# Optimization experiments

Measured on AMD Instinct MI355X. Metric: run time of the kernel, lower is better.

The kernel has to match this reference:

```python
import jax, jax.numpy as jnp
import numpy as np

EMB = 128
BINS = 32
CUT = 5.0
NLAYER = 5
NHID = 4  # extra hidden linears in edge MLP (hidden_dim_list has 5 entries total)
N_NODES = 50000
N_EDGES = 800000
N_GRAPH = 256
NODE_CLASS = 100


def setup_inputs() -> dict:
    key = jax.random.key(0)
    ks = jax.random.split(key, 20)
    s = 0.02
    inp = {
        'z': jax.random.randint(ks[0], (N_NODES,), 0, NODE_CLASS),
        'pos': jax.random.normal(ks[1], (N_NODES, 3), dtype=jnp.float32) * 3.0,
        'batch': jnp.sort(jax.random.randint(ks[2], (N_NODES,), 0, N_GRAPH)),
        'edge_index': jax.random.randint(ks[3], (2, N_EDGES), 0, N_NODES),
        # parameters
        'atom_table': jax.random.normal(ks[4], (NODE_CLASS, EMB), dtype=jnp.float32) * s,
        'atom_w': jax.random.normal(ks[5], (EMB, EMB), dtype=jnp.float32) * s,
        'atom_b': jnp.zeros((EMB,), jnp.float32),
        'edge_emb_w': jax.random.normal(ks[6], (BINS, EMB), dtype=jnp.float32) * s,
        'edge_emb_b': jnp.zeros((EMB,), jnp.float32),
        'edge_w0': jax.random.normal(ks[7], (NLAYER, 3 * EMB, EMB), dtype=jnp.float32) * s,
        'edge_b0': jnp.zeros((NLAYER, EMB), jnp.float32),
        'edge_w': jax.random.normal(ks[8], (NLAYER, NHID, EMB, EMB), dtype=jnp.float32) * s,
        'edge_b': jnp.zeros((NLAYER, NHID, EMB), jnp.float32),
        'node_w': jax.random.normal(ks[9], (NLAYER, EMB, EMB), dtype=jnp.float32) * s,
        'node_b': jnp.zeros((NLAYER, EMB), jnp.float32),
        'out_w': jax.random.normal(ks[10], (EMB, 1), dtype=jnp.float32) * s,
        'out_b': jnp.zeros((1,), jnp.float32),
    }
    return inp


def reference(z, pos, batch, edge_index, atom_table, atom_w, atom_b,
              edge_emb_w, edge_emb_b, edge_w0, edge_b0, edge_w, edge_b,
              node_w, node_b, out_w, out_b):
    silu = jax.nn.silu
    row, col = edge_index[0], edge_index[1]

    # atom embedding + linear
    h_node = atom_table[z] @ atom_w + atom_b  # [N, EMB]

    # edge distances -> gaussian basis expansion (linear spacing, log_base=1.0)
    d = jnp.linalg.norm(pos[row] - pos[col], axis=-1)  # [E]
    mu = jnp.linspace(0.0, CUT, BINS, dtype=jnp.float32)
    sigma = CUT / BINS
    basis = jnp.exp(-0.5 * ((d[:, None] - mu) / sigma) ** 2)  # [E, BINS]
    h_edge = basis @ edge_emb_w + edge_emb_b  # [E, EMB]

    # message passing layers
    for l in range(NLAYER):
        m = jnp.concatenate([h_edge, h_node[row], h_node[col]], axis=-1)  # [E, 3*EMB]
        m = silu(m @ edge_w0[l] + edge_b0[l])
        for k in range(NHID):
            m = silu(m @ edge_w[l, k] + edge_b[l, k])
        h_edge = h_edge + m  # residual edge update
        agg = jax.ops.segment_sum(h_edge, row, num_segments=N_NODES)  # [N, EMB]
        h_node = h_node + silu(agg @ node_w[l] + node_b[l])  # residual node update

    # scatter-mean graph pool
    sums = jax.ops.segment_sum(h_node, batch, num_segments=N_GRAPH)
    cnt = jax.ops.segment_sum(jnp.ones((h_node.shape[0],), h_node.dtype), batch, num_segments=N_GRAPH)
    h_graph = sums / jnp.clip(cnt, 1.0)[:, None]

    return h_graph @ out_w + out_b  # [N_GRAPH, 1]
```

## Files before the change

### kernel.cpp

```cpp
#include <hip/hip_runtime.h>

#define EMB      128
#define N_NODES_ 50000
#define N_EDGES_ 800000
#define N_GRAPH_ 256
#define NLAYER_  5

#define WP_ATOM  573440
#define WP_NODE0 589824
#define WP_EMB   671744
#define WP_TOTAL 675840

typedef short short8 __attribute__((ext_vector_type(8)));
typedef float floatx4 __attribute__((ext_vector_type(4)));

__device__ __forceinline__ float silu_f(float x) {
    return __fdividef(x, 1.0f + __expf(-x));
}
__device__ __forceinline__ float bf2f(unsigned short h) {
    return __uint_as_float(((unsigned)h) << 16);
}
__device__ __forceinline__ unsigned short f2bf(float f) {
    unsigned u = __float_as_uint(f);
    unsigned r = 0x7FFFu + ((u >> 16) & 1u);
    return (unsigned short)((u + r) >> 16);
}

#if defined(__has_builtin)
#if __has_builtin(__builtin_amdgcn_cvt_pk_bf16_f32)
#define HAVE_PK_BF16 1
#endif
#endif
#ifdef HAVE_PK_BF16
typedef __bf16 bf16x2 __attribute__((ext_vector_type(2)));
__device__ __forceinline__ unsigned f2bf_pk(float a, float b) {
    bf16x2 v = __builtin_amdgcn_cvt_pk_bf16_f32(a, b);
    unsigned u;
    __builtin_memcpy(&u, &v, 4);
    return u;
}
#else
__device__ __forceinline__ unsigned f2bf_pk(float a, float b) {
    return (unsigned)f2bf(a) | ((unsigned)f2bf(b) << 16);
}
#endif

__device__ __forceinline__ void wave_lds_fence() {
    __builtin_amdgcn_fence(__ATOMIC_ACQ_REL, "wavefront");
    __builtin_amdgcn_wave_barrier();
}

__global__ __launch_bounds__(256) void hist_kernel(
    const int* __restrict__ row, int* __restrict__ hist)
{
    const int e = blockIdx.x * 256 + threadIdx.x;
    if (e < N_EDGES_) atomicAdd(&hist[row[e]], 1);
}

__global__ __launch_bounds__(256) void scan_kernel(
    const int* __restrict__ hist, int* __restrict__ cursor)
{
    __shared__ int ssum[256];
    const int tid = threadIdx.x;
    const int chunk = (N_NODES_ + 255) / 256;
    const int base = tid * chunk;
    int s = 0;
    for (int i = 0; i < chunk; ++i) {
        const int idx = base + i;
        if (idx < N_NODES_) s += hist[idx];
    }
    ssum[tid] = s;
    __syncthreads();
    for (int off = 1; off < 256; off <<= 1) {
        const int t2 = (tid >= off) ? ssum[tid - off] : 0;
        __syncthreads();
        ssum[tid] += t2;
        __syncthreads();
    }
    int run = ssum[tid] - s;
    for (int i = 0; i < chunk; ++i) {
        const int idx = base + i;
        if (idx < N_NODES_) { cursor[idx] = run; run += hist[idx]; }
    }
}

__global__ __launch_bounds__(256) void scatter_kernel(
    const int* __restrict__ row, const int* __restrict__ col,
    int* __restrict__ cursor, int* __restrict__ row_s, int* __restrict__ col_s)
{
    const int e = blockIdx.x * 256 + threadIdx.x;
    if (e >= N_EDGES_) return;
    const int r = row[e];
    const int p = atomicAdd(&cursor[r], 1);
    row_s[p] = r;
    col_s[p] = col[e];
}

__global__ __launch_bounds__(256) void pack_w_kernel(
    const float* __restrict__ edge_w0, const float* __restrict__ edge_w,
    const float* __restrict__ atom_w, const float* __restrict__ node_w,
    const float* __restrict__ edge_emb_w,
    unsigned short* __restrict__ Wp)
{
    const int bid = blockIdx.x;
    int Kb, t;
    const float* src;
    unsigned short* dst;
    if (bid < 200) {
        const int l = bid / 40, r = bid % 40, s = r / 8;
        t = r % 8;
        Kb = (s == 0) ? 12 : 4;
        src = (s == 0) ? edge_w0 + (size_t)l * 384 * 128
                       : edge_w + ((size_t)l * 4 + (s - 1)) * 128 * 128;
        dst = Wp + (size_t)l * 114688 + ((s == 0) ? 0 : (49152 + (s - 1) * 16384))
            + (size_t)t * Kb * 512;
    } else if (bid < 208) {
        t = bid - 200; Kb = 4; src = atom_w;
        dst = Wp + WP_ATOM + (size_t)t * Kb * 512;
    } else if (bid < 248) {
        const int l = (bid - 208) >> 3; t = (bid - 208) & 7; Kb = 4;
        src = node_w + (size_t)l * 128 * 128;
        dst = Wp + WP_NODE0 + (size_t)l * 16384 + (size_t)t * Kb * 512;
    } else {
        t = bid - 248; Kb = 1; src = edge_emb_w;
        dst = Wp + WP_EMB + (size_t)t * 512;
    }
    const int n = Kb * 512;
    for (int p = threadIdx.x; p < n; p += 256) {
        const int j = p & 7, lane = (p >> 3) & 63, kb = p >> 9;
        const int k  = kb * 32 + ((lane >> 4) << 3) + j;
        const int nn = t * 16 + (lane & 15);
        dst[p] = f2bf(src[(size_t)k * 128 + nn]);
    }
}

__global__ __launch_bounds__(256, 3) void edge_mlp_csr_kernel(
    const unsigned short* __restrict__ h_node_bf, unsigned short* __restrict__ h_edge,
    const int* __restrict__ row_s, const int* __restrict__ col_s,
    const unsigned short* __restrict__ Wp,
    const float* __restrict__ b0, const float* __restrict__ bh)
{
    __shared__ __align__(16) unsigned short A[64][392];
    const int tid = threadIdx.x;
    const int e0 = blockIdx.x * 64;

    short8 he_reg[4];

    {
        const int t = tid >> 2, q = tid & 3;
        const int rg = row_s[e0 + t];
        const int cg = col_s[e0 + t];
        const unsigned short* pe = &h_edge[(size_t)(e0 + t) * 128];
        const unsigned short* pr = &h_node_bf[(size_t)rg * 128];
        const unsigned short* pc = &h_node_bf[(size_t)cg * 128];
#pragma unroll
        for (int i = 0; i < 12; ++i) {
            const int ch = q + 4 * i;
            const int k8 = ch << 3;
            const unsigned short* src = (ch < 16) ? (pe + k8)
                                      : (ch < 32) ? (pr + (k8 - 128))
                                                  : (pc + (k8 - 256));
            const short8 v = *(const short8*)src;
            if (i < 4) he_reg[i] = v;
            *(short8*)&A[t][k8] = v;
        }
    }
    __syncthreads();

    const int lane = tid & 63;
    const int wv   = tid >> 6;
    const int lr   = lane & 15;
    const int lg   = lane >> 4;
    const int nt0  = 2 * wv, nt1 = nt0 + 1;

    for (int s = 0; s < 5; ++s) {
        const int Kb   = (s == 0) ? 12 : 4;
        const int inb  = (s == 0) ? 0 : ((s & 1) ? 128 : 0);
        const int outb = (s & 1) ? 0 : 128;
        const unsigned short* __restrict__ Ws =
            Wp + ((s == 0) ? 0 : (49152 + (s - 1) * 16384));
        const float* __restrict__ bias = (s == 0) ? b0 : (bh + (s - 1) * 128);

        const float4 bv0 = *(const float4*)&bias[nt0 * 16 + lg * 4];
        const float4 bv1 = *(const float4*)&bias[nt1 * 16 + lg * 4];
        floatx4 acc0[4], acc1[4];
#pragma unroll
        for (int et = 0; et < 4; ++et) {
            acc0[et] = (floatx4){bv0.x, bv0.y, bv0.z, bv0.w};
            acc1[et] = (floatx4){bv1.x, bv1.y, bv1.z, bv1.w};
        }

        const unsigned short* aptr0 = Ws + ((size_t)(nt0 * Kb) * 64 + lane) * 8;
        const unsigned short* aptr1 = Ws + ((size_t)(nt1 * Kb) * 64 + lane) * 8;
#pragma unroll 2
        for (int kb = 0; kb < Kb; ++kb) {
            const short8 wf0 = *(const short8*)(aptr0 + (size_t)kb * 512);
            const short8 wf1 = *(const short8*)(aptr1 + (size_t)kb * 512);
#pragma unroll
            for (int et = 0; et < 4; ++et) {
                const short8 mf = *(const short8*)&A[et * 16 + lr][inb + kb * 32 + lg * 8];
                acc0[et] = __builtin_amdgcn_mfma_f32_16x16x32_bf16(wf0, mf, acc0[et], 0, 0, 0);
                acc1[et] = __builtin_amdgcn_mfma_f32_16x16x32_bf16(wf1, mf, acc1[et], 0, 0, 0);
            }
        }
        if (s == 0) __syncthreads();
#pragma unroll
        for (int et = 0; et < 4; ++et) {
            uint2 p0, p1;
            p0.x = f2bf_pk(silu_f(acc0[et][0]), silu_f(acc0[et][1]));
            p0.y = f2bf_pk(silu_f(acc0[et][2]), silu_f(acc0[et][3]));
            p1.x = f2bf_pk(silu_f(acc1[et][0]), silu_f(acc1[et][1]));
            p1.y = f2bf_pk(silu_f(acc1[et][2]), silu_f(acc1[et][3]));
            *(uint2*)&A[et * 16 + lr][outb + nt0 * 16 + lg * 4] = p0;
            *(uint2*)&A[et * 16 + lr][outb + nt1 * 16 + lg * 4] = p1;
        }
        __syncthreads();
    }

    {
        const int t = tid >> 2, q = tid & 3;
        unsigned short* pe = &h_edge[(size_t)(e0 + t) * 128];
#pragma unroll
        for (int i = 0; i < 4; ++i) {
            const int k8 = (q + 4 * i) << 3;
            const short8 mv = *(const short8*)&A[t][128 + k8];
            const short8 ov = he_reg[i];
            float he[8];
#pragma unroll
            for (int j = 0; j < 8; ++j)
                he[j] = bf2f((unsigned short)ov[j]) + bf2f((unsigned short)mv[j]);
            uint4 sv;
            sv.x = f2bf_pk(he[0], he[1]);
            sv.y = f2bf_pk(he[2], he[3]);
            sv.z = f2bf_pk(he[4], he[5]);
            sv.w = f2bf_pk(he[6], he[7]);
            *(uint4*)(pe + k8) = sv;
        }
    }
}

__global__ __launch_bounds__(256, 4) void node_agg_gemm_kernel(
    const unsigned short* __restrict__ h_edge,
    const int* __restrict__ hist, const int* __restrict__ cur_end,
    const unsigned short* __restrict__ Wpm, const float* __restrict__ bias,
    unsigned short* __restrict__ h_node_bf, int N)
{
    __shared__ __align__(16) unsigned short B[64][136];
    const int tid  = threadIdx.x;
    const int lane = tid & 63;
    const int wv   = tid >> 6;
    const int n0   = blockIdx.x * 64;

    {
        const int t = tid >> 2, q = tid & 3;
        const int n = n0 + t;
        float a[32];
#pragma unroll
        for (int j = 0; j < 32; ++j) a[j] = 0.f;
        if (n < N) {
            const int e_end = cur_end[n];
            const int e_beg = e_end - hist[n];
            for (int e = e_beg; e < e_end; ++e) {
                const unsigned short* p = &h_edge[(size_t)e * 128 + q * 32];
#pragma unroll
                for (int g = 0; g < 4; ++g) {
                    const short8 v = *(const short8*)(p + g * 8);
#pragma unroll
                    for (int j = 0; j < 8; ++j)
                        a[g * 8 + j] += bf2f((unsigned short)v[j]);
                }
            }
        }
#pragma unroll
        for (int g = 0; g < 4; ++g) {
            uint4 pk;
            pk.x = f2bf_pk(a[g * 8 + 0], a[g * 8 + 1]);
            pk.y = f2bf_pk(a[g * 8 + 2], a[g * 8 + 3]);
            pk.z = f2bf_pk(a[g * 8 + 4], a[g * 8 + 5]);
            pk.w = f2bf_pk(a[g * 8 + 6], a[g * 8 + 7]);
            *(uint4*)&B[t][q * 32 + g * 8] = pk;
        }
    }
    wave_lds_fence();

    const int lr = lane & 15, lg = lane >> 4;
    floatx4 acc[8];
#pragma unroll
    for (int nt = 0; nt < 8; ++nt) {
        const float4 bv = *(const float4*)&bias[nt * 16 + lg * 4];
        acc[nt] = (floatx4){bv.x, bv.y, bv.z, bv.w};
    }
    const unsigned short* brow = &B[wv * 16 + lr][0];
#pragma unroll 2
    for (int kb = 0; kb < 4; ++kb) {
        const short8 mf = *(const short8*)(brow + kb * 32 + lg * 8);
#pragma unroll
        for (int nt = 0; nt < 8; ++nt) {
            const short8 wf = *(const short8*)(Wpm + ((size_t)(nt * 4 + kb) * 64 + lane) * 8);
            acc[nt] = __builtin_amdgcn_mfma_f32_16x16x32_bf16(wf, mf, acc[nt], 0, 0, 0);
        }
    }
    const int node = n0 + wv * 16 + lr;
    if (node < N) {
        unsigned short* drow = &h_node_bf[(size_t)node * 128];
#pragma unroll
        for (int nt = 0; nt < 8; ++nt) {
            float x0 = silu_f(acc[nt][0]), x1 = silu_f(acc[nt][1]);
            float x2 = silu_f(acc[nt][2]), x3 = silu_f(acc[nt][3]);
            unsigned short* p = drow + nt * 16 + lg * 4;
            const uint2 d = *(const uint2*)p;
            x0 += bf2f((unsigned short)(d.x & 0xFFFF));
            x1 += bf2f((unsigned short)(d.x >> 16));
            x2 += bf2f((unsigned short)(d.y & 0xFFFF));
            x3 += bf2f((unsigned short)(d.y >> 16));
            uint2 o;
            o.x = f2bf_pk(x0, x1);
            o.y = f2bf_pk(x2, x3);
            *(uint2*)p = o;
        }
    }
}

__global__ __launch_bounds__(256, 4) void atom_gemm_mfma_kernel(
    const float* __restrict__ src, const int* __restrict__ gidx,
    const unsigned short* __restrict__ Wpm, const float* __restrict__ bias,
    unsigned short* __restrict__ dst, int N)
{
    __shared__ __align__(16) unsigned short B[64][136];
    const int tid  = threadIdx.x;
    const int lane = tid & 63;
    const int wv   = tid >> 6;
    const int n0   = blockIdx.x * 64;

    {
        const int t = tid >> 2, q = tid & 3;
        const int node = n0 + t;
        const float* srow = src;
        if (node < N) srow = &src[(size_t)gidx[node] * 128];
#pragma unroll
        for (int i = 0; i < 4; ++i) {
            const int k8 = (q + 4 * i) << 3;
            uint4 pk = make_uint4(0, 0, 0, 0);
            if (node < N) {
                const float4 f0 = *(const float4*)(srow + k8);
                const float4 f1 = *(const float4*)(srow + k8 + 4);
                pk.x = f2bf_pk(f0.x, f0.y);
                pk.y = f2bf_pk(f0.z, f0.w);
                pk.z = f2bf_pk(f1.x, f1.y);
                pk.w = f2bf_pk(f1.z, f1.w);
            }
            *(uint4*)&B[t][k8] = pk;
        }
    }
    wave_lds_fence();

    const int lr = lane & 15, lg = lane >> 4;
    floatx4 acc[8];
#pragma unroll
    for (int nt = 0; nt < 8; ++nt) {
        const float4 bv = *(const float4*)&bias[nt * 16 + lg * 4];
        acc[nt] = (floatx4){bv.x, bv.y, bv.z, bv.w};
    }
    const unsigned short* brow = &B[wv * 16 + lr][0];
#pragma unroll 2
    for (int kb = 0; kb < 4; ++kb) {
        const short8 mf = *(const short8*)(brow + kb * 32 + lg * 8);
#pragma unroll
        for (int nt = 0; nt < 8; ++nt) {
            const short8 wf = *(const short8*)(Wpm + ((size_t)(nt * 4 + kb) * 64 + lane) * 8);
            acc[nt] = __builtin_amdgcn_mfma_f32_16x16x32_bf16(wf, mf, acc[nt], 0, 0, 0);
        }
    }
    const int node = n0 + wv * 16 + lr;
    if (node < N) {
        unsigned short* drow = &dst[(size_t)node * 128];
#pragma unroll
        for (int nt = 0; nt < 8; ++nt) {
            uint2 o;
            o.x = f2bf_pk(acc[nt][0], acc[nt][1]);
            o.y = f2bf_pk(acc[nt][2], acc[nt][3]);
            *(uint2*)(drow + nt * 16 + lg * 4) = o;
        }
    }
}

__global__ __launch_bounds__(256, 4) void edge_embed_mfma_kernel(
    const float* __restrict__ pos, const int* __restrict__ row, const int* __restrict__ col,
    const unsigned short* __restrict__ Wpe, const float* __restrict__ bemb,
    unsigned short* __restrict__ h_edge)
{
    __shared__ __align__(16) unsigned short Bas[64][40];
    const int tid  = threadIdx.x;
    const int lane = tid & 63;
    const int wv   = tid >> 6;
    const int e0   = blockIdx.x * 64;

    {
        const int t = tid >> 2, q = tid & 3;
        const int rr = row[e0 + t], cc = col[e0 + t];
        const float dx = pos[rr * 3 + 0] - pos[cc * 3 + 0];
        const float dy = pos[rr * 3 + 1] - pos[cc * 3 + 1];
        const float dz = pos[rr * 3 + 2] - pos[cc * 3 + 2];
        const float d = sqrtf(dx * dx + dy * dy + dz * dz);
        const float invs = 32.0f / 5.0f;
        float e[8];
#pragma unroll
        for (int j = 0; j < 8; ++j) {
            const float mu = (float)(q * 8 + j) * (5.0f / 31.0f);
            const float tt = (d - mu) * invs;
            e[j] = __expf(-0.5f * tt * tt);
        }
        uint4 pk;
        pk.x = f2bf_pk(e[0], e[1]);
        pk.y = f2bf_pk(e[2], e[3]);
        pk.z = f2bf_pk(e[4], e[5]);
        pk.w = f2bf_pk(e[6], e[7]);
        *(uint4*)&Bas[t][q * 8] = pk;
    }
    wave_lds_fence();

    const int lr = lane & 15, lg = lane >> 4;
    floatx4 acc[8];
#pragma unroll
    for (int nt = 0; nt < 8; ++nt) {
        const float4 bv = *(const float4*)&bemb[nt * 16 + lg * 4];
        acc[nt] = (floatx4){bv.x, bv.y, bv.z, bv.w};
    }
    const short8 mf = *(const short8*)&Bas[wv * 16 + lr][lg * 8];
#pragma unroll
    for (int nt = 0; nt < 8; ++nt) {
        const short8 wf = *(const short8*)(Wpe + ((size_t)nt * 64 + lane) * 8);
        acc[nt] = __builtin_amdgcn_mfma_f32_16x16x32_bf16(wf, mf, acc[nt], 0, 0, 0);
    }
    unsigned short* erow = &h_edge[(size_t)(e0 + wv * 16 + lr) * 128];
#pragma unroll
    for (int nt = 0; nt < 8; ++nt) {
        uint2 o;
        o.x = f2bf_pk(acc[nt][0], acc[nt][1]);
        o.y = f2bf_pk(acc[nt][2], acc[nt][3]);
        *(uint2*)(erow + nt * 16 + lg * 4) = o;
    }
}

__global__ __launch_bounds__(128) void pool_kernel(
    const unsigned short* __restrict__ h_node_bf, const int* __restrict__ batch,
    float* __restrict__ sums, float* __restrict__ cnt, int N)
{
    __shared__ int bb[256];
    const int tid = threadIdx.x;
    const int n0 = blockIdx.x * 256;
    for (int idx = tid; idx < 256; idx += 128) {
        int n = n0 + idx;
        bb[idx] = (n < N) ? batch[n] : -1;
    }
    __syncthreads();
    int cur = bb[0];
    float run = 0.f, runc = 0.f;
    for (int i = 0; i < 256; ++i) {
        const int b = bb[i];
        if (b < 0) break;
        if (b != cur) {
            atomicAdd(&sums[(size_t)cur * 128 + tid], run);
            if (tid == 0) atomicAdd(&cnt[cur], runc);
            run = 0.f; runc = 0.f; cur = b;
        }
        run += bf2f(h_node_bf[(size_t)(n0 + i) * 128 + tid]);
        runc += 1.f;
    }
    atomicAdd(&sums[(size_t)cur * 128 + tid], run);
    if (tid == 0) atomicAdd(&cnt[cur], runc);
}

__global__ __launch_bounds__(256) void final_kernel(
    const float* __restrict__ sums, const float* __restrict__ cnt,
    const float* __restrict__ out_w, const float* __restrict__ out_b,
    float* __restrict__ out)
{
    const int g = threadIdx.x;
    const float c = fmaxf(cnt[g], 1.0f);
    float acc = 0.f;
    for (int jj = 0; jj < 128; ++jj) acc = fmaf(sums[(size_t)g * 128 + jj], out_w[jj], acc);
    out[g] = acc / c + out_b[0];
}

__global__ void zero_out_kernel(float* out, int n) {
    int i = blockIdx.x * 256 + threadIdx.x;
    if (i < n) out[i] = 0.f;
}


extern "C" void kernel_launch(void* const* d_in, const int* in_sizes, int n_in,
                              void* d_out, int out_size, void* d_ws, size_t ws_size,
                              hipStream_t stream)
{
    const int*   z          = (const int*)  d_in[0];
    const float* pos        = (const float*)d_in[1];
    const int*   batch      = (const int*)  d_in[2];
    const int*   eidx       = (const int*)  d_in[3];
    const float* atom_table = (const float*)d_in[4];
    const float* atom_w     = (const float*)d_in[5];
    const float* atom_b     = (const float*)d_in[6];
    const float* edge_emb_w = (const float*)d_in[7];
    const float* edge_emb_b = (const float*)d_in[8];
    const float* edge_w0    = (const float*)d_in[9];
    const float* edge_b0    = (const float*)d_in[10];
    const float* edge_w     = (const float*)d_in[11];
    const float* edge_b     = (const float*)d_in[12];
    const float* node_w     = (const float*)d_in[13];
    const float* node_b     = (const float*)d_in[14];
    const float* out_w      = (const float*)d_in[15];
    const float* out_b      = (const float*)d_in[16];
    const int* row = eidx;
    const int* col = eidx + N_EDGES_;

    float* aggb = (float*)d_ws;
    float* sums = aggb + (size_t)N_NODES_ * EMB;
    float* cnt  = sums + (size_t)N_GRAPH_ * EMB;
    unsigned short* h_node_bf = (unsigned short*)(cnt + N_GRAPH_);
    unsigned short* h_edge    = h_node_bf + (size_t)N_NODES_ * EMB;
    unsigned short* Wp        = h_edge + (size_t)N_EDGES_ * EMB;
    int* hist   = (int*)(Wp + WP_TOTAL);
    int* cursor = hist + N_NODES_;
    int* row_s  = cursor + N_NODES_;
    int* col_s  = row_s + N_EDGES_;

    const size_t need = ((size_t)(N_NODES_ * EMB + N_GRAPH_ * EMB + N_GRAPH_)) * 4
                      + ((size_t)N_NODES_ * EMB + (size_t)N_EDGES_ * EMB + (size_t)WP_TOTAL) * 2
                      + ((size_t)N_NODES_ * 2 + (size_t)N_EDGES_ * 2) * 4;

    if (ws_size < need) {
        zero_out_kernel<<<1, 256, 0, stream>>>((float*)d_out, N_GRAPH_);
        return;
    }

    const int grid_rows64 = (N_NODES_ + 63) / 64;

    (void)hipMemsetAsync(hist, 0, N_NODES_ * sizeof(int), stream);
    hist_kernel<<<(N_EDGES_ + 255) / 256, 256, 0, stream>>>(row, hist);
    scan_kernel<<<1, 256, 0, stream>>>(hist, cursor);
    scatter_kernel<<<(N_EDGES_ + 255) / 256, 256, 0, stream>>>(row, col, cursor, row_s, col_s);

    pack_w_kernel<<<256, 256, 0, stream>>>(edge_w0, edge_w, atom_w, node_w, edge_emb_w, Wp);

    atom_gemm_mfma_kernel<<<grid_rows64, 256, 0, stream>>>(
        atom_table, z, Wp + WP_ATOM, atom_b, h_node_bf, N_NODES_);
    edge_embed_mfma_kernel<<<N_EDGES_ / 64, 256, 0, stream>>>(
        pos, row_s, col_s, Wp + WP_EMB, edge_emb_b, h_edge);

    for (int l = 0; l < NLAYER_; ++l) {
        edge_mlp_csr_kernel<<<N_EDGES_ / 64, 256, 0, stream>>>(
            h_node_bf, h_edge, row_s, col_s,
            Wp + (size_t)l * 114688,
            edge_b0 + (size_t)l * 128, edge_b + (size_t)l * 4 * 128);
        node_agg_gemm_kernel<<<grid_rows64, 256, 0, stream>>>(
            h_edge, hist, cursor,
            Wp + WP_NODE0 + (size_t)l * 16384, node_b + (size_t)l * 128,
            h_node_bf, N_NODES_);
    }

    (void)hipMemsetAsync(sums, 0, ((size_t)N_GRAPH_ * EMB + N_GRAPH_) * sizeof(float), stream);
    pool_kernel<<<(N_NODES_ + 255) / 256, 128, 0, stream>>>(h_node_bf, batch, sums, cnt, N_NODES_);
    final_kernel<<<1, 256, 0, stream>>>(sums, cnt, out_w, out_b, (float*)d_out);
}
```

Before: 2.519 ms.

## Stream edge MLP first-layer operands from global memory and shrink shared buffers

The edge MLP kernel no longer stages the concatenated [h_edge, h_node[row], h_node[col]] tile in a 64x392 shared array. The first layer instead reads its MFMA B-fragments directly from global memory, and the hidden layers ping-pong through two smaller 64x136 shared buffers. The residual add is fused into the last layer's epilogue by re-reading h_edge, and occupancy is raised to 4 blocks per SM. This cuts LDS use and a staging pass and sync, but trades them for uncoalesced per-lane global gathers inside the MFMA loop and a second read of h_edge.

```diff
diff --git a/kernel.cpp b/kernel.cpp
--- a/kernel.cpp
+++ b/kernel.cpp
@@ -134,76 +134,59 @@
     }
 }
 
-__global__ __launch_bounds__(256, 3) void edge_mlp_csr_kernel(
+__global__ __launch_bounds__(256, 4) void edge_mlp_csr_kernel(
     const unsigned short* __restrict__ h_node_bf, unsigned short* __restrict__ h_edge,
     const int* __restrict__ row_s, const int* __restrict__ col_s,
     const unsigned short* __restrict__ Wp,
     const float* __restrict__ b0, const float* __restrict__ bh)
 {
-    __shared__ __align__(16) unsigned short A[64][392];
-    const int tid = threadIdx.x;
-    const int e0 = blockIdx.x * 64;
-
-    short8 he_reg[4];
-
-    {
-        const int t = tid >> 2, q = tid & 3;
-        const int rg = row_s[e0 + t];
-        const int cg = col_s[e0 + t];
-        const unsigned short* pe = &h_edge[(size_t)(e0 + t) * 128];
-        const unsigned short* pr = &h_node_bf[(size_t)rg * 128];
-        const unsigned short* pc = &h_node_bf[(size_t)cg * 128];
-#pragma unroll
-        for (int i = 0; i < 12; ++i) {
-            const int ch = q + 4 * i;
-            const int k8 = ch << 3;
-            const unsigned short* src = (ch < 16) ? (pe + k8)
-                                      : (ch < 32) ? (pr + (k8 - 128))
-                                                  : (pc + (k8 - 256));
-            const short8 v = *(const short8*)src;
-            if (i < 4) he_reg[i] = v;
-            *(short8*)&A[t][k8] = v;
-        }
-    }
-    __syncthreads();
-
+    __shared__ __align__(16) unsigned short P[2][64][136];
+
+    const int tid  = threadIdx.x;
+    const int e0   = blockIdx.x * 64;
     const int lane = tid & 63;
     const int wv   = tid >> 6;
     const int lr   = lane & 15;
     const int lg   = lane >> 4;
     const int nt0  = 2 * wv, nt1 = nt0 + 1;
 
-    for (int s = 0; s < 5; ++s) {
-        const int Kb   = (s == 0) ? 12 : 4;
-        const int inb  = (s == 0) ? 0 : ((s & 1) ? 128 : 0);
-        const int outb = (s & 1) ? 0 : 128;
-        const unsigned short* __restrict__ Ws =
-            Wp + ((s == 0) ? 0 : (49152 + (s - 1) * 16384));
-        const float* __restrict__ bias = (s == 0) ? b0 : (bh + (s - 1) * 128);
-
-        const float4 bv0 = *(const float4*)&bias[nt0 * 16 + lg * 4];
-        const float4 bv1 = *(const float4*)&bias[nt1 * 16 + lg * 4];
-        floatx4 acc0[4], acc1[4];
+    int eoff[4], roff[4], coff[4];
+#pragma unroll
+    for (int et = 0; et < 4; ++et) {
+        const int e = e0 + et * 16 + lr;
+        eoff[et] = e * 128 + lg * 8;
+        roff[et] = row_s[e] * 128 + lg * 8;
+        coff[et] = col_s[e] * 128 + lg * 8;
+    }
+
+    floatx4 acc0[4], acc1[4];
+
+    {
+        const float4 bv0 = *(const float4*)&b0[nt0 * 16 + lg * 4];
+        const float4 bv1 = *(const float4*)&b0[nt1 * 16 + lg * 4];
 #pragma unroll
         for (int et = 0; et < 4; ++et) {
             acc0[et] = (floatx4){bv0.x, bv0.y, bv0.z, bv0.w};
             acc1[et] = (floatx4){bv1.x, bv1.y, bv1.z, bv1.w};
         }
-
-        const unsigned short* aptr0 = Ws + ((size_t)(nt0 * Kb) * 64 + lane) * 8;
-        const unsigned short* aptr1 = Ws + ((size_t)(nt1 * Kb) * 64 + lane) * 8;
-#pragma unroll 2
-        for (int kb = 0; kb < Kb; ++kb) {
+        const unsigned short* aptr0 = Wp + ((size_t)(nt0 * 12) * 64 + lane) * 8;
+        const unsigned short* aptr1 = Wp + ((size_t)(nt1 * 12) * 64 + lane) * 8;
+#pragma unroll
+        for (int kb = 0; kb < 12; ++kb) {
             const short8 wf0 = *(const short8*)(aptr0 + (size_t)kb * 512);
             const short8 wf1 = *(const short8*)(aptr1 + (size_t)kb * 512);
+            const int off = (kb & 3) * 32;
 #pragma unroll
             for (int et = 0; et < 4; ++et) {
-                const short8 mf = *(const short8*)&A[et * 16 + lr][inb + kb * 32 + lg * 8];
+                const unsigned short* src =
+                    (kb < 4) ? (h_edge + eoff[et])
+                  : (kb < 8) ? (h_node_bf + roff[et])
+                             : (h_node_bf + coff[et]);
+                const short8 mf = *(const short8*)(src + off);
                 acc0[et] = __builtin_amdgcn_mfma_f32_16x16x32_bf16(wf0, mf, acc0[et], 0, 0, 0);
                 acc1[et] = __builtin_amdgcn_mfma_f32_16x16x32_bf16(wf1, mf, acc1[et], 0, 0, 0);
             }
         }
-        if (s == 0) __syncthreads();
 #pragma unroll
         for (int et = 0; et < 4; ++et) {
             uint2 p0, p1;
@@ -211,30 +194,71 @@
             p0.y = f2bf_pk(silu_f(acc0[et][2]), silu_f(acc0[et][3]));
             p1.x = f2bf_pk(silu_f(acc1[et][0]), silu_f(acc1[et][1]));
             p1.y = f2bf_pk(silu_f(acc1[et][2]), silu_f(acc1[et][3]));
-            *(uint2*)&A[et * 16 + lr][outb + nt0 * 16 + lg * 4] = p0;
-            *(uint2*)&A[et * 16 + lr][outb + nt1 * 16 + lg * 4] = p1;
-        }
-        __syncthreads();
-    }
-
-    {
-        const int t = tid >> 2, q = tid & 3;
-        unsigned short* pe = &h_edge[(size_t)(e0 + t) * 128];
-#pragma unroll
-        for (int i = 0; i < 4; ++i) {
-            const int k8 = (q + 4 * i) << 3;
-            const short8 mv = *(const short8*)&A[t][128 + k8];
-            const short8 ov = he_reg[i];
-            float he[8];
-#pragma unroll
-            for (int j = 0; j < 8; ++j)
-                he[j] = bf2f((unsigned short)ov[j]) + bf2f((unsigned short)mv[j]);
-            uint4 sv;
-            sv.x = f2bf_pk(he[0], he[1]);
-            sv.y = f2bf_pk(he[2], he[3]);
-            sv.z = f2bf_pk(he[4], he[5]);
-            sv.w = f2bf_pk(he[6], he[7]);
-            *(uint4*)(pe + k8) = sv;
+            *(uint2*)&P[0][et * 16 + lr][nt0 * 16 + lg * 4] = p0;
+            *(uint2*)&P[0][et * 16 + lr][nt1 * 16 + lg * 4] = p1;
+        }
+    }
+    __syncthreads();
+
+#pragma unroll 1
+    for (int s = 1; s < 5; ++s) {
+        const int inb  = (s - 1) & 1;
+        const int outb = s & 1;
+        const unsigned short* __restrict__ Ws = Wp + 49152 + (size_t)(s - 1) * 16384;
+        const float* __restrict__ bias = bh + (size_t)(s - 1) * 128;
+
+        const float4 bv0 = *(const float4*)&bias[nt0 * 16 + lg * 4];
+        const float4 bv1 = *(const float4*)&bias[nt1 * 16 + lg * 4];
+#pragma unroll
+        for (int et = 0; et < 4; ++et) {
+            acc0[et] = (floatx4){bv0.x, bv0.y, bv0.z, bv0.w};
+            acc1[et] = (floatx4){bv1.x, bv1.y, bv1.z, bv1.w};
+        }
+        const unsigned short* aptr0 = Ws + ((size_t)(nt0 * 4) * 64 + lane) * 8;
+        const unsigned short* aptr1 = Ws + ((size_t)(nt1 * 4) * 64 + lane) * 8;
+#pragma unroll 2
+        for (int kb = 0; kb < 4; ++kb) {
+            const short8 wf0 = *(const short8*)(aptr0 + (size_t)kb * 512);
+            const short8 wf1 = *(const short8*)(aptr1 + (size_t)kb * 512);
+#pragma unroll
+            for (int et = 0; et < 4; ++et) {
+                const short8 mf = *(const short8*)&P[inb][et * 16 + lr][kb * 32 + lg * 8];
+                acc0[et] = __builtin_amdgcn_mfma_f32_16x16x32_bf16(wf0, mf, acc0[et], 0, 0, 0);
+                acc1[et] = __builtin_amdgcn_mfma_f32_16x16x32_bf16(wf1, mf, acc1[et], 0, 0, 0);
+            }
+        }
+        if (s < 4) {
+#pragma unroll
+            for (int et = 0; et < 4; ++et) {
+                uint2 p0, p1;
+                p0.x = f2bf_pk(silu_f(acc0[et][0]), silu_f(acc0[et][1]));
+                p0.y = f2bf_pk(silu_f(acc0[et][2]), silu_f(acc0[et][3]));
+                p1.x = f2bf_pk(silu_f(acc1[et][0]), silu_f(acc1[et][1]));
+                p1.y = f2bf_pk(silu_f(acc1[et][2]), silu_f(acc1[et][3]));
+                *(uint2*)&P[outb][et * 16 + lr][nt0 * 16 + lg * 4] = p0;
+                *(uint2*)&P[outb][et * 16 + lr][nt1 * 16 + lg * 4] = p1;
+            }
+            __syncthreads();
+        } else {
+#pragma unroll
+            for (int et = 0; et < 4; ++et) {
+                unsigned short* erow = h_edge + (size_t)(e0 + et * 16 + lr) * 128;
+                const uint2 d0 = *(const uint2*)(erow + nt0 * 16 + lg * 4);
+                const uint2 d1 = *(const uint2*)(erow + nt1 * 16 + lg * 4);
+                float x0 = silu_f(acc0[et][0]) + bf2f((unsigned short)(d0.x & 0xFFFF));
+                float x1 = silu_f(acc0[et][1]) + bf2f((unsigned short)(d0.x >> 16));
+                float x2 = silu_f(acc0[et][2]) + bf2f((unsigned short)(d0.y & 0xFFFF));
+                float x3 = silu_f(acc0[et][3]) + bf2f((unsigned short)(d0.y >> 16));
+                float y0 = silu_f(acc1[et][0]) + bf2f((unsigned short)(d1.x & 0xFFFF));
+                float y1 = silu_f(acc1[et][1]) + bf2f((unsigned short)(d1.x >> 16));
+                float y2 = silu_f(acc1[et][2]) + bf2f((unsigned short)(d1.y & 0xFFFF));
+                float y3 = silu_f(acc1[et][3]) + bf2f((unsigned short)(d1.y >> 16));
+                uint2 o0, o1;
+                o0.x = f2bf_pk(x0, x1); o0.y = f2bf_pk(x2, x3);
+                o1.x = f2bf_pk(y0, y1); o1.y = f2bf_pk(y2, y3);
+                *(uint2*)(erow + nt0 * 16 + lg * 4) = o0;
+                *(uint2*)(erow + nt1 * 16 + lg * 4) = o1;
+            }
         }
     }
 }
```

Measured after the change: 2.796 ms. 11.0% more time.
